# Performance work log

Hardware: AMD Instinct MI355X
Metric: run time of the kernel (lower is better)

## Reference

```python
import jax, jax.numpy as jnp
import numpy as np

N = 16384
D = 128

def setup_inputs() -> dict:
    key = jax.random.key(0)
    k1, k2 = jax.random.split(key)
    point_cloud1 = jax.random.normal(k1, (1, N, D), dtype=jnp.float32)
    point_cloud2 = jax.random.normal(k2, (1, N, D), dtype=jnp.float32)
    return {"point_cloud1": point_cloud1, "point_cloud2": point_cloud2}

def reference(point_cloud1, point_cloud2):
    # Squared pairwise distances via the expansion ||a-b||^2 = ||a||^2 + ||b||^2 - 2 a.b
    # (mathematically identical to the original broadcast-subtract form, but avoids
    #  materializing the [1, N, N, D] intermediate).
    a2 = jnp.sum(point_cloud1 * point_cloud1, axis=-1)          # [1, N]
    b2 = jnp.sum(point_cloud2 * point_cloud2, axis=-1)          # [1, N]
    ab = jnp.einsum('bnd,bmd->bnm', point_cloud1, point_cloud2) # [1, N, N]
    dists_squared = a2[:, :, None] + b2[:, None, :] - 2.0 * ab  # [1, N, N]
    min_dists1 = jnp.min(dists_squared, axis=2)  # nearest in cloud2 for each point in cloud1
    min_dists2 = jnp.min(dists_squared, axis=1)  # nearest in cloud1 for each point in cloud2
    return jnp.mean(min_dists1) + jnp.mean(min_dists2)
```

## Files before the change

### kernel.cpp

```cpp
#include <hip/hip_runtime.h>
#include <hip/hip_bf16.h>

#define N_PTS 16384
#define DIM   128

typedef __bf16 bf16x8 __attribute__((ext_vector_type(8)));
typedef float  f32x4  __attribute__((ext_vector_type(4)));

__device__ __forceinline__ unsigned fmap(float f) {
    unsigned u = __float_as_uint(f);
    return (u & 0x80000000u) ? ~u : (u | 0x80000000u);
}
__device__ __forceinline__ float funmap(unsigned u) {
    return __uint_as_float((u & 0x80000000u) ? (u & 0x7FFFFFFFu) : ~u);
}

__device__ __forceinline__ void gload_lds16(const void* g, void* l) {
    __builtin_amdgcn_global_load_lds(
        (const __attribute__((address_space(1))) void*)g,
        (__attribute__((address_space(3))) void*)l, 16, 0, 0);
}

__global__ void chamfer_prep2(const float* __restrict__ A, const float* __restrict__ B,
                              unsigned short* __restrict__ Abf, unsigned short* __restrict__ Bbf,
                              float* __restrict__ a2, float* __restrict__ b2,
                              unsigned* __restrict__ rowmin, unsigned* __restrict__ colmin) {
    int wave = blockIdx.x * 4 + (threadIdx.x >> 6);
    int lane = threadIdx.x & 63;
    int isB  = wave >= N_PTS;
    int row  = isB ? (wave - N_PTS) : wave;
    const float* src = isB ? B : A;
    unsigned short* dst = isB ? Bbf : Abf;

    float2 v = *reinterpret_cast<const float2*>(&src[(size_t)row * DIM + lane * 2]);

    __bf16 bx = (__bf16)v.x, by = (__bf16)v.y;
    ushort2 st;
    st.x = __builtin_bit_cast(unsigned short, bx);
    st.y = __builtin_bit_cast(unsigned short, by);
    *reinterpret_cast<ushort2*>(&dst[(size_t)row * DIM + lane * 2]) = st;

    float s = fmaf(v.x, v.x, v.y * v.y);
    #pragma unroll
    for (int off = 32; off; off >>= 1) s += __shfl_down(s, off);
    if (lane == 0) {
        if (isB) { b2[row] = s; colmin[row] = 0xFFFFFFFFu; }
        else     { a2[row] = s; rowmin[row] = 0xFFFFFFFFu; }
    }
}

__global__ __launch_bounds__(512, 2)
void chamfer_gemm_min3(const unsigned short* __restrict__ Abf, const unsigned short* __restrict__ Bbf,
                       const float* __restrict__ a2, const float* __restrict__ b2,
                       unsigned* __restrict__ rowmin, unsigned* __restrict__ colmin) {
    __shared__ __align__(16) unsigned char sA[65536];
    __shared__ __align__(16) unsigned char sB[2][32768];

    const int b = blockIdx.x;
    const int tm_base = (b >> 2) * 256;
    const int tn0 = (b & 3) * 32;

    const int t = threadIdx.x;
    const int w = t >> 6, lane = t & 63;
    const int lq = lane >> 4, lr = lane & 15;
    const int wr = (w >> 1) * 64;
    const int wc = (w & 1) * 64;

    #pragma unroll
    for (int j = 0; j < 8; ++j) {
        int chunk = ((w << 3) + j) * 64 + lane;
        int r = chunk >> 4, kc = (chunk & 15) ^ (r & 7);
        gload_lds16(Abf + (size_t)(tm_base + r) * DIM + kc * 8, sA + chunk * 16);
    }
    #pragma unroll
    for (int j = 0; j < 4; ++j) {
        int chunk = ((w << 2) + j) * 64 + lane;
        int r = chunk >> 4, kc = (chunk & 15) ^ (r & 7);
        gload_lds16(Bbf + (size_t)(tn0 * 128 + r) * DIM + kc * 8, sB[0] + chunk * 16);
    }

    float a2v[4][4];
    #pragma unroll
    for (int mi = 0; mi < 4; ++mi) {
        float4 q = *reinterpret_cast<const float4*>(&a2[tm_base + wr + mi * 16 + lq * 4]);
        a2v[mi][0] = q.x; a2v[mi][1] = q.y; a2v[mi][2] = q.z; a2v[mi][3] = q.w;
    }

    __syncthreads();

    for (int it = 0; it < 32; ++it) {
        const int cur = it & 1;
        const int tn = tn0 + it;

        if (it + 1 < 32) {
            #pragma unroll
            for (int j = 0; j < 4; ++j) {
                int chunk = ((w << 2) + j) * 64 + lane;
                int r = chunk >> 4, kc = (chunk & 15) ^ (r & 7);
                gload_lds16(Bbf + (size_t)((tn + 1) * 128 + r) * DIM + kc * 8,
                            sB[cur ^ 1] + chunk * 16);
            }
        }

        f32x4 acc[4][4] = {};
        #pragma unroll
        for (int ks = 0; ks < 4; ++ks) {
            const int kc = ks * 4 + lq;
            bf16x8 af[4], bfr[4];
            #pragma unroll
            for (int mi = 0; mi < 4; ++mi) {
                int r = wr + mi * 16 + lr;
                af[mi] = *reinterpret_cast<const bf16x8*>(&sA[r * 256 + ((kc * 16) ^ ((r & 7) << 4))]);
            }
            #pragma unroll
            for (int ni = 0; ni < 4; ++ni) {
                int r = wc + ni * 16 + lr;
                bfr[ni] = *reinterpret_cast<const bf16x8*>(&sB[cur][r * 256 + ((kc * 16) ^ ((r & 7) << 4))]);
            }
            #pragma unroll
            for (int mi = 0; mi < 4; ++mi)
                #pragma unroll
                for (int ni = 0; ni < 4; ++ni)
                    acc[mi][ni] = __builtin_amdgcn_mfma_f32_16x16x32_bf16(af[mi], bfr[ni], acc[mi][ni], 0, 0, 0);
        }

        const int col_base = tn * 128 + wc;
        float b2v[4];
        #pragma unroll
        for (int ni = 0; ni < 4; ++ni) b2v[ni] = b2[col_base + ni * 16 + lr];

        float v[16];
        #pragma unroll
        for (int mi = 0; mi < 4; ++mi) {
            #pragma unroll
            for (int j = 0; j < 4; ++j) {
                float m = fmaf(-2.f, acc[mi][0][j], b2v[0]);
                m = fminf(m, fmaf(-2.f, acc[mi][1][j], b2v[1]));
                m = fminf(m, fmaf(-2.f, acc[mi][2][j], b2v[2]));
                m = fminf(m, fmaf(-2.f, acc[mi][3][j], b2v[3]));
                v[mi * 4 + j] = m;
            }
        }
        #pragma unroll
        for (int k = 0; k < 8; ++k) {
            float s = (lr & 8) ? v[k] : v[k + 8];
            float r = __shfl_xor(s, 8);
            v[k] = (lr & 8) ? fminf(v[k + 8], r) : fminf(v[k], r);
        }
        #pragma unroll
        for (int k = 0; k < 4; ++k) {
            float s = (lr & 4) ? v[k] : v[k + 4];
            float r = __shfl_xor(s, 4);
            v[k] = (lr & 4) ? fminf(v[k + 4], r) : fminf(v[k], r);
        }
        #pragma unroll
        for (int k = 0; k < 2; ++k) {
            float s = (lr & 2) ? v[k] : v[k + 2];
            float r = __shfl_xor(s, 2);
            v[k] = (lr & 2) ? fminf(v[k + 2], r) : fminf(v[k], r);
        }
        {
            float s = (lr & 1) ? v[0] : v[1];
            float r = __shfl_xor(s, 1);
            v[0] = (lr & 1) ? fminf(v[1], r) : fminf(v[0], r);
        }
        const int own_row = tm_base + wr + ((lr >> 2) << 4) + (lq << 2) + (lr & 3);

        float cp[4];
        #pragma unroll
        for (int ni = 0; ni < 4; ++ni) {
            float m = fmaf(-2.f, acc[0][ni][0], a2v[0][0]);
            #pragma unroll
            for (int mi = 0; mi < 4; ++mi)
                #pragma unroll
                for (int j = 0; j < 4; ++j)
                    if (mi | j) m = fminf(m, fmaf(-2.f, acc[mi][ni][j], a2v[mi][j]));
            cp[ni] = m;
        }
        #pragma unroll
        for (int k = 0; k < 2; ++k) {
            float s = (lane & 16) ? cp[k] : cp[k + 2];
            float r = __shfl_xor(s, 16);
            cp[k] = (lane & 16) ? fminf(cp[k + 2], r) : fminf(cp[k], r);
        }
        float cfin;
        {
            float s = (lane & 32) ? cp[0] : cp[1];
            float r = __shfl_xor(s, 32);
            cfin = (lane & 32) ? fminf(cp[1], r) : fminf(cp[0], r);
        }
        const int ni_own = ((lq & 1) << 1) | (lq >> 1);
        const int own_col = col_base + ni_own * 16 + lr;

        __syncthreads();

        atomicMin(&rowmin[own_row], fmap(v[0]));
        atomicMin(&colmin[own_col], fmap(cfin));
    }
}

__global__ void chamfer_finalize2(const unsigned* __restrict__ rowmin,
                                  const unsigned* __restrict__ colmin,
                                  const float* __restrict__ a2, const float* __restrict__ b2,
                                  float* __restrict__ out) {
    __shared__ double sred[16];
    int t = threadIdx.x;
    double s = 0.0;
    for (int i = t; i < N_PTS; i += 1024)
        s += ((double)funmap(rowmin[i]) + (double)a2[i])
           + ((double)funmap(colmin[i]) + (double)b2[i]);
    #pragma unroll
    for (int off = 32; off; off >>= 1) s += __shfl_down(s, off);
    if ((t & 63) == 0) sred[t >> 6] = s;
    __syncthreads();
    if (t == 0) {
        double tot = 0.0;
        #pragma unroll
        for (int i = 0; i < 16; ++i) tot += sred[i];
        out[0] = (float)(tot * (1.0 / (double)N_PTS));
    }
}

__global__ void chamfer_prep_fb(const float* __restrict__ A, const float* __restrict__ B,
                                float* __restrict__ a2, float* __restrict__ b2,
                                unsigned* __restrict__ rowmin, unsigned* __restrict__ colmin) {
    int wave = blockIdx.x * 4 + (threadIdx.x >> 6);
    int lane = threadIdx.x & 63;
    int isB  = wave >= N_PTS;
    int row  = isB ? (wave - N_PTS) : wave;
    const float* src = isB ? B : A;
    float2 v = *reinterpret_cast<const float2*>(&src[(size_t)row * DIM + lane * 2]);
    float s = v.x * v.x + v.y * v.y;
    #pragma unroll
    for (int off = 32; off; off >>= 1) s += __shfl_down(s, off);
    if (lane == 0) {
        if (isB) { b2[row] = s; colmin[row] = 0xFFFFFFFFu; }
        else     { a2[row] = s; rowmin[row] = 0xFFFFFFFFu; }
    }
}

__global__ __launch_bounds__(256, 2)
void chamfer_gemm_min_fb(const float* __restrict__ A, const float* __restrict__ B,
                         const float* __restrict__ a2, const float* __restrict__ b2,
                         unsigned* __restrict__ rowmin, unsigned* __restrict__ colmin) {
    __shared__ __align__(16) unsigned char sA[32768];
    __shared__ __align__(16) unsigned char sB[32768];

    const int t = threadIdx.x;
    const int tile_m = blockIdx.y * 128;
    const int tile_n = blockIdx.x * 128;

    #pragma unroll
    for (int it = 0; it < 8; ++it) {
        int c  = it * 256 + t;
        int r  = c >> 4;
        int kc = c & 15;
        int lds_off = r * 256 + ((kc * 16) ^ ((r & 7) << 4));
        {
            const float4* p = reinterpret_cast<const float4*>(&A[(size_t)(tile_m + r) * DIM + kc * 8]);
            float4 u = p[0], vv = p[1];
            bf16x8 wv;
            wv[0]=(__bf16)u.x; wv[1]=(__bf16)u.y; wv[2]=(__bf16)u.z; wv[3]=(__bf16)u.w;
            wv[4]=(__bf16)vv.x; wv[5]=(__bf16)vv.y; wv[6]=(__bf16)vv.z; wv[7]=(__bf16)vv.w;
            *reinterpret_cast<bf16x8*>(&sA[lds_off]) = wv;
        }
        {
            const float4* p = reinterpret_cast<const float4*>(&B[(size_t)(tile_n + r) * DIM + kc * 8]);
            float4 u = p[0], vv = p[1];
            bf16x8 wv;
            wv[0]=(__bf16)u.x; wv[1]=(__bf16)u.y; wv[2]=(__bf16)u.z; wv[3]=(__bf16)u.w;
            wv[4]=(__bf16)vv.x; wv[5]=(__bf16)vv.y; wv[6]=(__bf16)vv.z; wv[7]=(__bf16)vv.w;
            *reinterpret_cast<bf16x8*>(&sB[lds_off]) = wv;
        }
    }
    __syncthreads();

    const int w  = t >> 6, lane = t & 63;
    const int wr = (w >> 1) * 64;
    const int wc = (w & 1) * 64;
    const int lq = lane >> 4, lr = lane & 15;

    f32x4 acc[4][4] = {};
    #pragma unroll
    for (int ks = 0; ks < 4; ++ks) {
        const int kc = ks * 4 + lq;
        bf16x8 af[4], bfr[4];
        #pragma unroll
        for (int mi = 0; mi < 4; ++mi) {
            int r = wr + mi * 16 + lr;
            af[mi] = *reinterpret_cast<const bf16x8*>(&sA[r * 256 + ((kc * 16) ^ ((r & 7) << 4))]);
        }
        #pragma unroll
        for (int ni = 0; ni < 4; ++ni) {
            int r = wc + ni * 16 + lr;
            bfr[ni] = *reinterpret_cast<const bf16x8*>(&sB[r * 256 + ((kc * 16) ^ ((r & 7) << 4))]);
        }
        #pragma unroll
        for (int mi = 0; mi < 4; ++mi)
            #pragma unroll
            for (int ni = 0; ni < 4; ++ni)
                acc[mi][ni] = __builtin_amdgcn_mfma_f32_16x16x32_bf16(af[mi], bfr[ni], acc[mi][ni], 0, 0, 0);
    }

    float b2v[4];
    #pragma unroll
    for (int ni = 0; ni < 4; ++ni) b2v[ni] = b2[tile_n + wc + ni * 16 + lr];
    float a2v[4][4];
    #pragma unroll
    for (int mi = 0; mi < 4; ++mi)
        #pragma unroll
        for (int j = 0; j < 4; ++j) a2v[mi][j] = a2[tile_m + wr + mi * 16 + lq * 4 + j];

    float rmin[4][4];
    #pragma unroll
    for (int mi = 0; mi < 4; ++mi) {
        #pragma unroll
        for (int j = 0; j < 4; ++j) {
            float m0 = fminf(fmaf(-2.f, acc[mi][0][j], b2v[0]), fmaf(-2.f, acc[mi][1][j], b2v[1]));
            float m1 = fminf(fmaf(-2.f, acc[mi][2][j], b2v[2]), fmaf(-2.f, acc[mi][3][j], b2v[3]));
            float m  = fminf(m0, m1);
            #pragma unroll
            for (int off = 1; off < 16; off <<= 1) m = fminf(m, __shfl_xor(m, off));
            rmin[mi][j] = m + a2v[mi][j];
        }
    }

    float cmin[4];
    #pragma unroll
    for (int ni = 0; ni < 4; ++ni) {
        float m = fmaf(-2.f, acc[0][ni][0], a2v[0][0]);
        #pragma unroll
        for (int mi = 0; mi < 4; ++mi)
            #pragma unroll
            for (int j = 0; j < 4; ++j)
                if (mi | j) m = fminf(m, fmaf(-2.f, acc[mi][ni][j], a2v[mi][j]));
        m = fminf(m, __shfl_xor(m, 16));
        m = fminf(m, __shfl_xor(m, 32));
        cmin[ni] = m + b2v[ni];
    }

    __syncthreads();
    unsigned* rmin_s = reinterpret_cast<unsigned*>(sA);
    unsigned* cmin_s = rmin_s + 128;
    reinterpret_cast<unsigned*>(sA)[t] = 0xFFFFFFFFu;
    __syncthreads();

    if (lr == 0) {
        #pragma unroll
        for (int mi = 0; mi < 4; ++mi)
            #pragma unroll
            for (int j = 0; j < 4; ++j)
                atomicMin(&rmin_s[wr + mi * 16 + lq * 4 + j], fmap(rmin[mi][j]));
    }
    if (lq == 0) {
        #pragma unroll
        for (int ni = 0; ni < 4; ++ni)
            atomicMin(&cmin_s[wc + ni * 16 + lr], fmap(cmin[ni]));
    }
    __syncthreads();

    if (t < 128) atomicMin(&rowmin[tile_m + t], rmin_s[t]);
    else         atomicMin(&colmin[tile_n + t - 128], cmin_s[t - 128]);
}

__global__ void chamfer_finalize_fb(const unsigned* __restrict__ rowmin,
                                    const unsigned* __restrict__ colmin,
                                    float* __restrict__ out) {
    __shared__ double sred[16];
    int t = threadIdx.x;
    double s = 0.0;
    for (int i = t; i < N_PTS; i += 1024)
        s += (double)funmap(rowmin[i]) + (double)funmap(colmin[i]);
    #pragma unroll
    for (int off = 32; off; off >>= 1) s += __shfl_down(s, off);
    if ((t & 63) == 0) sred[t >> 6] = s;
    __syncthreads();
    if (t == 0) {
        double tot = 0.0;
        #pragma unroll
        for (int i = 0; i < 16; ++i) tot += sred[i];
        out[0] = (float)(tot * (1.0 / (double)N_PTS));
    }
}

extern "C" void kernel_launch(void* const* d_in, const int* in_sizes, int n_in,
                              void* d_out, int out_size, void* d_ws, size_t ws_size,
                              hipStream_t stream) {
    const float* A = (const float*)d_in[0];
    const float* B = (const float*)d_in[1];
    float* out = (float*)d_out;
    char* ws = (char*)d_ws;

    const size_t BF = (size_t)N_PTS * DIM * sizeof(unsigned short);
    const size_t need = 2 * BF + 4 * (size_t)(1 << 16);

    if (ws_size >= need) {
        unsigned short* Abf = (unsigned short*)(ws);
        unsigned short* Bbf = (unsigned short*)(ws + BF);
        float*    a2     = (float*)(ws + 2 * BF);
        float*    b2     = (float*)(ws + 2 * BF + (1 << 16));
        unsigned* rowmin = (unsigned*)(ws + 2 * BF + (2 << 16));
        unsigned* colmin = (unsigned*)(ws + 2 * BF + (3 << 16));

        chamfer_prep2<<<(2 * N_PTS) / 4, 256, 0, stream>>>(A, B, Abf, Bbf, a2, b2, rowmin, colmin);
        chamfer_gemm_min3<<<256, 512, 0, stream>>>(Abf, Bbf, a2, b2, rowmin, colmin);
        chamfer_finalize2<<<1, 1024, 0, stream>>>(rowmin, colmin, a2, b2, out);
    } else {
        float*    a2     = (float*)(ws);
        float*    b2     = (float*)(ws + (1 << 16));
        unsigned* rowmin = (unsigned*)(ws + (2 << 16));
        unsigned* colmin = (unsigned*)(ws + (3 << 16));

        chamfer_prep_fb<<<(2 * N_PTS) / 4, 256, 0, stream>>>(A, B, a2, b2, rowmin, colmin);
        dim3 grid(N_PTS / 128, N_PTS / 128);
        chamfer_gemm_min_fb<<<grid, 256, 0, stream>>>(A, B, a2, b2, rowmin, colmin);
        chamfer_finalize_fb<<<1, 1024, 0, stream>>>(rowmin, colmin, out);
    }
}
```

Before: 119.6 us.

## Fold squared norms into augmented-K GEMM and keep A fragments in registers

Extends the bf16 operands from K=128 to K=160, adding hi/lo bf16 splits of the squared norms and ones columns, with A pre-scaled by -2. The MFMA output then equals the full distance, and the epilogue drops the per-element FMA with norm terms. A fragments now stay in registers instead of LDS, the block shrinks to 256 threads, and row minima are accumulated per thread across all tiles. Row and column minima go to two partial buffers merged in finalize. This adds 25% more MFMA work and relies on the hi/lo bf16 split to keep enough precision in the norms.

```diff
diff --git a/kernel.cpp b/kernel.cpp
--- a/kernel.cpp
+++ b/kernel.cpp
@@ -3,6 +3,8 @@
 
 #define N_PTS 16384
 #define DIM   128
+#define KAUG  160
+#define ROWB  (KAUG * 2)
 
 typedef __bf16 bf16x8 __attribute__((ext_vector_type(8)));
 typedef float  f32x4  __attribute__((ext_vector_type(4)));
@@ -19,6 +21,205 @@
     __builtin_amdgcn_global_load_lds(
         (const __attribute__((address_space(1))) void*)g,
         (__attribute__((address_space(3))) void*)l, 16, 0, 0);
+}
+
+__global__ void chamfer_prep4(const float* __restrict__ A, const float* __restrict__ B,
+                              unsigned short* __restrict__ Ax, unsigned short* __restrict__ Bx,
+                              unsigned* __restrict__ minbuf) {
+    int gtid = blockIdx.x * 256 + threadIdx.x;
+    if (gtid < 4 * N_PTS) minbuf[gtid] = 0xFFFFFFFFu;
+
+    int wave = blockIdx.x * 4 + (threadIdx.x >> 6);
+    int lane = threadIdx.x & 63;
+    int isB  = wave >= N_PTS;
+    int row  = isB ? (wave - N_PTS) : wave;
+    const float* src = isB ? B : A;
+    unsigned short* dst = isB ? Bx : Ax;
+
+    float2 v = *reinterpret_cast<const float2*>(&src[(size_t)row * DIM + lane * 2]);
+
+    float sc = isB ? 1.f : -2.f;
+    __bf16 bx = (__bf16)(sc * v.x), by = (__bf16)(sc * v.y);
+    ushort2 st;
+    st.x = __builtin_bit_cast(unsigned short, bx);
+    st.y = __builtin_bit_cast(unsigned short, by);
+    *reinterpret_cast<ushort2*>(&dst[(size_t)row * KAUG + lane * 2]) = st;
+
+    float s = fmaf(v.x, v.x, v.y * v.y);
+    #pragma unroll
+    for (int off = 1; off < 64; off <<= 1) s += __shfl_xor(s, off);
+
+    __bf16 hb = (__bf16)s;
+    float  hf = (float)hb;
+    __bf16 lb = (__bf16)(s - hf);
+    unsigned short hu = __builtin_bit_cast(unsigned short, hb);
+    unsigned short lu = __builtin_bit_cast(unsigned short, lb);
+    const unsigned short one = 0x3F80;
+
+    if (lane < 16) {
+        ushort2 tw; tw.x = 0; tw.y = 0;
+        if (lane == 0) { tw.x = isB ? hu : one; tw.y = isB ? lu : one; }
+        if (lane == 1) { tw.x = isB ? one : hu; tw.y = isB ? one : lu; }
+        *reinterpret_cast<ushort2*>(&dst[(size_t)row * KAUG + 128 + lane * 2]) = tw;
+    }
+}
+
+__global__ __launch_bounds__(256, 2)
+void chamfer_gemm_min4(const unsigned short* __restrict__ Ax,
+                       const unsigned short* __restrict__ Bx,
+                       unsigned* __restrict__ rowminS,
+                       unsigned* __restrict__ colminS) {
+    __shared__ __align__(16) unsigned char sB[2][40960];
+
+    const int b   = blockIdx.x;
+    const int tm  = (b >> 2) * 128;
+    const int tn0 = (b & 3) * 32;
+
+    const int t = threadIdx.x, w = t >> 6, lane = t & 63;
+    const int lq = lane >> 4, lr = lane & 15;
+    const int wr = (w >> 1) * 64, wc = (w & 1) * 64;
+
+    bf16x8 af[4][5];
+    #pragma unroll
+    for (int mi = 0; mi < 4; ++mi)
+        #pragma unroll
+        for (int ks = 0; ks < 5; ++ks) {
+            int row = tm + wr + mi * 16 + lr;
+            int kc  = ks * 4 + lq;
+            af[mi][ks] = *reinterpret_cast<const bf16x8*>(&Ax[(size_t)row * KAUG + kc * 8]);
+        }
+
+    #pragma unroll
+    for (int j = 0; j < 10; ++j) {
+        int chunk = j * 256 + t;
+        int r = chunk / 20;
+        int s = chunk - r * 20;
+        int c = (s < 16) ? (s ^ (r & 7)) : (16 + ((s - 16) ^ (r & 3)));
+        gload_lds16(Bx + (size_t)(tn0 * 128 + r) * KAUG + c * 8, sB[0] + chunk * 16);
+    }
+    __syncthreads();
+
+    const int own_row = tm + wr + ((lr >> 2) << 4) + (lq << 2) + (lr & 3);
+    const int ni_own  = ((lq & 1) << 1) | (lq >> 1);
+    float rmin_run = 3.4e38f;
+
+    for (int it = 0; it < 32; ++it) {
+        const int cur = it & 1;
+        const int tn  = tn0 + it;
+
+        if (it + 1 < 32) {
+            #pragma unroll
+            for (int j = 0; j < 10; ++j) {
+                int chunk = j * 256 + t;
+                int r = chunk / 20;
+                int s = chunk - r * 20;
+                int c = (s < 16) ? (s ^ (r & 7)) : (16 + ((s - 16) ^ (r & 3)));
+                gload_lds16(Bx + (size_t)((tn + 1) * 128 + r) * KAUG + c * 8,
+                            sB[cur ^ 1] + chunk * 16);
+            }
+        }
+
+        f32x4 acc[4][4] = {};
+        #pragma unroll
+        for (int ks = 0; ks < 5; ++ks) {
+            bf16x8 bfr[4];
+            #pragma unroll
+            for (int ni = 0; ni < 4; ++ni) {
+                int r = wc + ni * 16 + lr;
+                int slot = (ks < 4) ? ((ks * 4 + lq) ^ (r & 7)) : (16 + (lq ^ (r & 3)));
+                bfr[ni] = *reinterpret_cast<const bf16x8*>(&sB[cur][r * ROWB + slot * 16]);
+            }
+            #pragma unroll
+            for (int mi = 0; mi < 4; ++mi)
+                #pragma unroll
+                for (int ni = 0; ni < 4; ++ni)
+                    acc[mi][ni] = __builtin_amdgcn_mfma_f32_16x16x32_bf16(af[mi][ks], bfr[ni], acc[mi][ni], 0, 0, 0);
+        }
+
+        float v[16];
+        #pragma unroll
+        for (int mi = 0; mi < 4; ++mi)
+            #pragma unroll
+            for (int j = 0; j < 4; ++j)
+                v[mi * 4 + j] = fminf(fminf(acc[mi][0][j], acc[mi][1][j]),
+                                      fminf(acc[mi][2][j], acc[mi][3][j]));
+        #pragma unroll
+        for (int k = 0; k < 8; ++k) {
+            float s = (lr & 8) ? v[k] : v[k + 8];
+            float r = __shfl_xor(s, 8);
+            v[k] = (lr & 8) ? fminf(v[k + 8], r) : fminf(v[k], r);
+        }
+        #pragma unroll
+        for (int k = 0; k < 4; ++k) {
+            float s = (lr & 4) ? v[k] : v[k + 4];
+            float r = __shfl_xor(s, 4);
+            v[k] = (lr & 4) ? fminf(v[k + 4], r) : fminf(v[k], r);
+        }
+        #pragma unroll
+        for (int k = 0; k < 2; ++k) {
+            float s = (lr & 2) ? v[k] : v[k + 2];
+            float r = __shfl_xor(s, 2);
+            v[k] = (lr & 2) ? fminf(v[k + 2], r) : fminf(v[k], r);
+        }
+        {
+            float s = (lr & 1) ? v[0] : v[1];
+            float r = __shfl_xor(s, 1);
+            v[0] = (lr & 1) ? fminf(v[1], r) : fminf(v[0], r);
+        }
+        rmin_run = fminf(rmin_run, v[0]);
+
+        float cp[4];
+        #pragma unroll
+        for (int ni = 0; ni < 4; ++ni) {
+            float m0 = fminf(fminf(acc[0][ni][0], acc[0][ni][1]), fminf(acc[0][ni][2], acc[0][ni][3]));
+            float m1 = fminf(fminf(acc[1][ni][0], acc[1][ni][1]), fminf(acc[1][ni][2], acc[1][ni][3]));
+            float m2 = fminf(fminf(acc[2][ni][0], acc[2][ni][1]), fminf(acc[2][ni][2], acc[2][ni][3]));
+            float m3 = fminf(fminf(acc[3][ni][0], acc[3][ni][1]), fminf(acc[3][ni][2], acc[3][ni][3]));
+            cp[ni] = fminf(fminf(m0, m1), fminf(m2, m3));
+        }
+        #pragma unroll
+        for (int k = 0; k < 2; ++k) {
+            float s = (lane & 16) ? cp[k] : cp[k + 2];
+            float r = __shfl_xor(s, 16);
+            cp[k] = (lane & 16) ? fminf(cp[k + 2], r) : fminf(cp[k], r);
+        }
+        float cfin;
+        {
+            float s = (lane & 32) ? cp[0] : cp[1];
+            float r = __shfl_xor(s, 32);
+            cfin = (lane & 32) ? fminf(cp[1], r) : fminf(cp[0], r);
+        }
+        const int own_col = tn * 128 + wc + ni_own * 16 + lr;
+
+        __syncthreads();
+
+        atomicMin(&colminS[(size_t)(w >> 1) * N_PTS + own_col], fmap(cfin));
+    }
+
+    atomicMin(&rowminS[(size_t)(w & 1) * N_PTS + own_row], fmap(rmin_run));
+}
+
+__global__ void chamfer_finalize4(const unsigned* __restrict__ rowminS,
+                                  const unsigned* __restrict__ colminS,
+                                  float* __restrict__ out) {
+    __shared__ double sred[16];
+    int t = threadIdx.x;
+    double s = 0.0;
+    for (int i = t; i < N_PTS; i += 1024) {
+        unsigned rm = min(rowminS[i], rowminS[i + N_PTS]);
+        unsigned cm = min(colminS[i], colminS[i + N_PTS]);
+        s += (double)funmap(rm) + (double)funmap(cm);
+    }
+    #pragma unroll
+    for (int off = 32; off; off >>= 1) s += __shfl_down(s, off);
+    if ((t & 63) == 0) sred[t >> 6] = s;
+    __syncthreads();
+    if (t == 0) {
+        double tot = 0.0;
+        #pragma unroll
+        for (int i = 0; i < 16; ++i) tot += sred[i];
+        out[0] = (float)(tot * (1.0 / (double)N_PTS));
+    }
 }
 
 __global__ void chamfer_prep2(const float* __restrict__ A, const float* __restrict__ B,
@@ -33,7 +234,6 @@
     unsigned short* dst = isB ? Bbf : Abf;
 
     float2 v = *reinterpret_cast<const float2*>(&src[(size_t)row * DIM + lane * 2]);
-
     __bf16 bx = (__bf16)v.x, by = (__bf16)v.y;
     ushort2 st;
     st.x = __builtin_bit_cast(unsigned short, bx);
@@ -54,7 +254,7 @@
                        const float* __restrict__ a2, const float* __restrict__ b2,
                        unsigned* __restrict__ rowmin, unsigned* __restrict__ colmin) {
     __shared__ __align__(16) unsigned char sA[65536];
-    __shared__ __align__(16) unsigned char sB[2][32768];
+    __shared__ __align__(16) unsigned char sB2[2][32768];
 
     const int b = blockIdx.x;
     const int tm_base = (b >> 2) * 256;
@@ -76,7 +276,7 @@
     for (int j = 0; j < 4; ++j) {
         int chunk = ((w << 2) + j) * 64 + lane;
         int r = chunk >> 4, kc = (chunk & 15) ^ (r & 7);
-        gload_lds16(Bbf + (size_t)(tn0 * 128 + r) * DIM + kc * 8, sB[0] + chunk * 16);
+        gload_lds16(Bbf + (size_t)(tn0 * 128 + r) * DIM + kc * 8, sB2[0] + chunk * 16);
     }
 
     float a2v[4][4];
@@ -85,7 +285,6 @@
         float4 q = *reinterpret_cast<const float4*>(&a2[tm_base + wr + mi * 16 + lq * 4]);
         a2v[mi][0] = q.x; a2v[mi][1] = q.y; a2v[mi][2] = q.z; a2v[mi][3] = q.w;
     }
-
     __syncthreads();
 
     for (int it = 0; it < 32; ++it) {
@@ -98,7 +297,7 @@
                 int chunk = ((w << 2) + j) * 64 + lane;
                 int r = chunk >> 4, kc = (chunk & 15) ^ (r & 7);
                 gload_lds16(Bbf + (size_t)((tn + 1) * 128 + r) * DIM + kc * 8,
-                            sB[cur ^ 1] + chunk * 16);
+                            sB2[cur ^ 1] + chunk * 16);
             }
         }
 
@@ -106,22 +305,22 @@
         #pragma unroll
         for (int ks = 0; ks < 4; ++ks) {
             const int kc = ks * 4 + lq;
-            bf16x8 af[4], bfr[4];
+            bf16x8 af2[4], bfr[4];
             #pragma unroll
             for (int mi = 0; mi < 4; ++mi) {
                 int r = wr + mi * 16 + lr;
-                af[mi] = *reinterpret_cast<const bf16x8*>(&sA[r * 256 + ((kc * 16) ^ ((r & 7) << 4))]);
+                af2[mi] = *reinterpret_cast<const bf16x8*>(&sA[r * 256 + ((kc * 16) ^ ((r & 7) << 4))]);
             }
             #pragma unroll
             for (int ni = 0; ni < 4; ++ni) {
                 int r = wc + ni * 16 + lr;
-                bfr[ni] = *reinterpret_cast<const bf16x8*>(&sB[cur][r * 256 + ((kc * 16) ^ ((r & 7) << 4))]);
+                bfr[ni] = *reinterpret_cast<const bf16x8*>(&sB2[cur][r * 256 + ((kc * 16) ^ ((r & 7) << 4))]);
             }
             #pragma unroll
             for (int mi = 0; mi < 4; ++mi)
                 #pragma unroll
                 for (int ni = 0; ni < 4; ++ni)
-                    acc[mi][ni] = __builtin_amdgcn_mfma_f32_16x16x32_bf16(af[mi], bfr[ni], acc[mi][ni], 0, 0, 0);
+                    acc[mi][ni] = __builtin_amdgcn_mfma_f32_16x16x32_bf16(af2[mi], bfr[ni], acc[mi][ni], 0, 0, 0);
         }
 
         const int col_base = tn * 128 + wc;
@@ -221,168 +420,6 @@
     }
 }
 
-__global__ void chamfer_prep_fb(const float* __restrict__ A, const float* __restrict__ B,
-                                float* __restrict__ a2, float* __restrict__ b2,
-                                unsigned* __restrict__ rowmin, unsigned* __restrict__ colmin) {
-    int wave = blockIdx.x * 4 + (threadIdx.x >> 6);
-    int lane = threadIdx.x & 63;
-    int isB  = wave >= N_PTS;
-    int row  = isB ? (wave - N_PTS) : wave;
-    const float* src = isB ? B : A;
-    float2 v = *reinterpret_cast<const float2*>(&src[(size_t)row * DIM + lane * 2]);
-    float s = v.x * v.x + v.y * v.y;
-    #pragma unroll
-    for (int off = 32; off; off >>= 1) s += __shfl_down(s, off);
-    if (lane == 0) {
-        if (isB) { b2[row] = s; colmin[row] = 0xFFFFFFFFu; }
-        else     { a2[row] = s; rowmin[row] = 0xFFFFFFFFu; }
-    }
-}
-
-__global__ __launch_bounds__(256, 2)
-void chamfer_gemm_min_fb(const float* __restrict__ A, const float* __restrict__ B,
-                         const float* __restrict__ a2, const float* __restrict__ b2,
-                         unsigned* __restrict__ rowmin, unsigned* __restrict__ colmin) {
-    __shared__ __align__(16) unsigned char sA[32768];
-    __shared__ __align__(16) unsigned char sB[32768];
-
-    const int t = threadIdx.x;
-    const int tile_m = blockIdx.y * 128;
-    const int tile_n = blockIdx.x * 128;
-
-    #pragma unroll
-    for (int it = 0; it < 8; ++it) {
-        int c  = it * 256 + t;
-        int r  = c >> 4;
-        int kc = c & 15;
-        int lds_off = r * 256 + ((kc * 16) ^ ((r & 7) << 4));
-        {
-            const float4* p = reinterpret_cast<const float4*>(&A[(size_t)(tile_m + r) * DIM + kc * 8]);
-            float4 u = p[0], vv = p[1];
-            bf16x8 wv;
-            wv[0]=(__bf16)u.x; wv[1]=(__bf16)u.y; wv[2]=(__bf16)u.z; wv[3]=(__bf16)u.w;
-            wv[4]=(__bf16)vv.x; wv[5]=(__bf16)vv.y; wv[6]=(__bf16)vv.z; wv[7]=(__bf16)vv.w;
-            *reinterpret_cast<bf16x8*>(&sA[lds_off]) = wv;
-        }
-        {
-            const float4* p = reinterpret_cast<const float4*>(&B[(size_t)(tile_n + r) * DIM + kc * 8]);
-            float4 u = p[0], vv = p[1];
-            bf16x8 wv;
-            wv[0]=(__bf16)u.x; wv[1]=(__bf16)u.y; wv[2]=(__bf16)u.z; wv[3]=(__bf16)u.w;
-            wv[4]=(__bf16)vv.x; wv[5]=(__bf16)vv.y; wv[6]=(__bf16)vv.z; wv[7]=(__bf16)vv.w;
-            *reinterpret_cast<bf16x8*>(&sB[lds_off]) = wv;
-        }
-    }
-    __syncthreads();
-
-    const int w  = t >> 6, lane = t & 63;
-    const int wr = (w >> 1) * 64;
-    const int wc = (w & 1) * 64;
-    const int lq = lane >> 4, lr = lane & 15;
-
-    f32x4 acc[4][4] = {};
-    #pragma unroll
-    for (int ks = 0; ks < 4; ++ks) {
-        const int kc = ks * 4 + lq;
-        bf16x8 af[4], bfr[4];
-        #pragma unroll
-        for (int mi = 0; mi < 4; ++mi) {
-            int r = wr + mi * 16 + lr;
-            af[mi] = *reinterpret_cast<const bf16x8*>(&sA[r * 256 + ((kc * 16) ^ ((r & 7) << 4))]);
-        }
-        #pragma unroll
-        for (int ni = 0; ni < 4; ++ni) {
-            int r = wc + ni * 16 + lr;
-            bfr[ni] = *reinterpret_cast<const bf16x8*>(&sB[r * 256 + ((kc * 16) ^ ((r & 7) << 4))]);
-        }
-        #pragma unroll
-        for (int mi = 0; mi < 4; ++mi)
-            #pragma unroll
-            for (int ni = 0; ni < 4; ++ni)
-                acc[mi][ni] = __builtin_amdgcn_mfma_f32_16x16x32_bf16(af[mi], bfr[ni], acc[mi][ni], 0, 0, 0);
-    }
-
-    float b2v[4];
-    #pragma unroll
-    for (int ni = 0; ni < 4; ++ni) b2v[ni] = b2[tile_n + wc + ni * 16 + lr];
-    float a2v[4][4];
-    #pragma unroll
-    for (int mi = 0; mi < 4; ++mi)
-        #pragma unroll
-        for (int j = 0; j < 4; ++j) a2v[mi][j] = a2[tile_m + wr + mi * 16 + lq * 4 + j];
-
-    float rmin[4][4];
-    #pragma unroll
-    for (int mi = 0; mi < 4; ++mi) {
-        #pragma unroll
-        for (int j = 0; j < 4; ++j) {
-            float m0 = fminf(fmaf(-2.f, acc[mi][0][j], b2v[0]), fmaf(-2.f, acc[mi][1][j], b2v[1]));
-            float m1 = fminf(fmaf(-2.f, acc[mi][2][j], b2v[2]), fmaf(-2.f, acc[mi][3][j], b2v[3]));
-            float m  = fminf(m0, m1);
-            #pragma unroll
-            for (int off = 1; off < 16; off <<= 1) m = fminf(m, __shfl_xor(m, off));
-            rmin[mi][j] = m + a2v[mi][j];
-        }
-    }
-
-    float cmin[4];
-    #pragma unroll
-    for (int ni = 0; ni < 4; ++ni) {
-        float m = fmaf(-2.f, acc[0][ni][0], a2v[0][0]);
-        #pragma unroll
-        for (int mi = 0; mi < 4; ++mi)
-            #pragma unroll
-            for (int j = 0; j < 4; ++j)
-                if (mi | j) m = fminf(m, fmaf(-2.f, acc[mi][ni][j], a2v[mi][j]));
-        m = fminf(m, __shfl_xor(m, 16));
-        m = fminf(m, __shfl_xor(m, 32));
-        cmin[ni] = m + b2v[ni];
-    }
-
-    __syncthreads();
-    unsigned* rmin_s = reinterpret_cast<unsigned*>(sA);
-    unsigned* cmin_s = rmin_s + 128;
-    reinterpret_cast<unsigned*>(sA)[t] = 0xFFFFFFFFu;
-    __syncthreads();
-
-    if (lr == 0) {
-        #pragma unroll
-        for (int mi = 0; mi < 4; ++mi)
-            #pragma unroll
-            for (int j = 0; j < 4; ++j)
-                atomicMin(&rmin_s[wr + mi * 16 + lq * 4 + j], fmap(rmin[mi][j]));
-    }
-    if (lq == 0) {
-        #pragma unroll
-        for (int ni = 0; ni < 4; ++ni)
-            atomicMin(&cmin_s[wc + ni * 16 + lr], fmap(cmin[ni]));
-    }
-    __syncthreads();
-
-    if (t < 128) atomicMin(&rowmin[tile_m + t], rmin_s[t]);
-    else         atomicMin(&colmin[tile_n + t - 128], cmin_s[t - 128]);
-}
-
-__global__ void chamfer_finalize_fb(const unsigned* __restrict__ rowmin,
-                                    const unsigned* __restrict__ colmin,
-                                    float* __restrict__ out) {
-    __shared__ double sred[16];
-    int t = threadIdx.x;
-    double s = 0.0;
-    for (int i = t; i < N_PTS; i += 1024)
-        s += (double)funmap(rowmin[i]) + (double)funmap(colmin[i]);
-    #pragma unroll
-    for (int off = 32; off; off >>= 1) s += __shfl_down(s, off);
-    if ((t & 63) == 0) sred[t >> 6] = s;
-    __syncthreads();
-    if (t == 0) {
-        double tot = 0.0;
-        #pragma unroll
-        for (int i = 0; i < 16; ++i) tot += sred[i];
-        out[0] = (float)(tot * (1.0 / (double)N_PTS));
-    }
-}
-
 extern "C" void kernel_launch(void* const* d_in, const int* in_sizes, int n_in,
                               void* d_out, int out_size, void* d_ws, size_t ws_size,
                               hipStream_t stream) {
@@ -391,10 +428,23 @@
     float* out = (float*)d_out;
     char* ws = (char*)d_ws;
 
-    const size_t BF = (size_t)N_PTS * DIM * sizeof(unsigned short);
-    const size_t need = 2 * BF + 4 * (size_t)(1 << 16);
-
-    if (ws_size >= need) {
+    const size_t SZ4   = (size_t)N_PTS * KAUG * sizeof(unsigned short);
+    const size_t need4 = 2 * SZ4 + 4 * (size_t)N_PTS * 4;
+
+    const size_t BF    = (size_t)N_PTS * DIM * sizeof(unsigned short);
+    const size_t need3 = 2 * BF + 4 * (size_t)(1 << 16);
+
+    if (ws_size >= need4) {
+        unsigned short* Ax = (unsigned short*)(ws);
+        unsigned short* Bx = (unsigned short*)(ws + SZ4);
+        unsigned* minbuf   = (unsigned*)(ws + 2 * SZ4);
+        unsigned* rowminS  = minbuf;
+        unsigned* colminS  = minbuf + 2 * N_PTS;
+
+        chamfer_prep4<<<(2 * N_PTS) / 4, 256, 0, stream>>>(A, B, Ax, Bx, minbuf);
+        chamfer_gemm_min4<<<512, 256, 0, stream>>>(Ax, Bx, rowminS, colminS);
+        chamfer_finalize4<<<1, 1024, 0, stream>>>(rowminS, colminS, out);
+    } else if (ws_size >= need3) {
         unsigned short* Abf = (unsigned short*)(ws);
         unsigned short* Bbf = (unsigned short*)(ws + BF);
         float*    a2     = (float*)(ws + 2 * BF);
@@ -405,15 +455,5 @@
         chamfer_prep2<<<(2 * N_PTS) / 4, 256, 0, stream>>>(A, B, Abf, Bbf, a2, b2, rowmin, colmin);
         chamfer_gemm_min3<<<256, 512, 0, stream>>>(Abf, Bbf, a2, b2, rowmin, colmin);
         chamfer_finalize2<<<1, 1024, 0, stream>>>(rowmin, colmin, a2, b2, out);
-    } else {
-        float*    a2     = (float*)(ws);
-        float*    b2     = (float*)(ws + (1 << 16));
-        unsigned* rowmin = (unsigned*)(ws + (2 << 16));
-        unsigned* colmin = (unsigned*)(ws + (3 << 16));
-
-        chamfer_prep_fb<<<(2 * N_PTS) / 4, 256, 0, stream>>>(A, B, a2, b2, rowmin, colmin);
-        dim3 grid(N_PTS / 128, N_PTS / 128);
-        chamfer_gemm_min_fb<<<grid, 256, 0, stream>>>(A, B, a2, b2, rowmin, colmin);
-        chamfer_finalize_fb<<<1, 1024, 0, stream>>>(rowmin, colmin, out);
-    }
-}
+    }
+}
```

After: 106.1 us. 11.3% less time.
